# Kernel optimization log

Hardware: AMD Instinct MI355X
Metric: run time of the kernel (lower is better)

The kernel has to match this reference:

```python
import jax, jax.numpy as jnp
import numpy as np

B, L, D, H = 1024, 128, 768, 256
EPS = 1e-5  # torch BatchNorm1d default eps


def _masked_mean(x, lens):
    # x: [B, L, D], lens: [B] int -> mean over first lens[i] rows per sample
    mask = (jnp.arange(x.shape[1])[None, :] < lens[:, None]).astype(x.dtype)  # [B, L]
    return jnp.einsum('bld,bl->bd', x, mask) / lens[:, None].astype(x.dtype)


def _batchnorm_train(x, gamma, beta):
    # training-mode BN: batch mean and biased variance
    mu = jnp.mean(x, axis=0)
    var = jnp.mean((x - mu) ** 2, axis=0)
    return gamma * (x - mu) / jnp.sqrt(var + EPS) + beta


def setup_inputs() -> dict:
    key = jax.random.key(0)
    ks = jax.random.split(key, 12)
    user_features = jax.random.normal(ks[0], (B, L, D), jnp.float32)
    hashtag_features = jax.random.normal(ks[1], (B, L, D), jnp.float32)
    user_lens = jax.random.randint(ks[2], (B,), 1, L + 1, jnp.int32)
    hashtag_lens = jax.random.randint(ks[3], (B,), 1, L + 1, jnp.int32)
    def lin(k, fan_out, fan_in):
        bound = 1.0 / np.sqrt(fan_in)
        kw, kb = jax.random.split(k)
        w = jax.random.uniform(kw, (fan_out, fan_in), jnp.float32, -bound, bound)
        b = jax.random.uniform(kb, (fan_out,), jnp.float32, -bound, bound)
        return w, b
    fc1_w, fc1_b = lin(ks[4], D, 2 * D)
    fc2_w, fc2_b = lin(ks[5], H, D)
    fc3_w, fc3_b = lin(ks[6], 1, H)
    bn1_g = jnp.ones((D,), jnp.float32)
    bn1_b = jnp.zeros((D,), jnp.float32)
    bn2_g = jnp.ones((H,), jnp.float32)
    bn2_b = jnp.zeros((H,), jnp.float32)
    return {
        'user_features': user_features, 'hashtag_features': hashtag_features,
        'user_lens': user_lens, 'hashtag_lens': hashtag_lens,
        'fc1_w': fc1_w, 'fc1_b': fc1_b, 'bn1_g': bn1_g, 'bn1_b': bn1_b,
        'fc2_w': fc2_w, 'fc2_b': fc2_b, 'bn2_g': bn2_g, 'bn2_b': bn2_b,
        'fc3_w': fc3_w, 'fc3_b': fc3_b,
    }


def reference(user_features, hashtag_features, user_lens, hashtag_lens,
              fc1_w, fc1_b, bn1_g, bn1_b, fc2_w, fc2_b, bn2_g, bn2_b,
              fc3_w, fc3_b):
    # fused ragged mean pooling (replaces per-sample python loop)
    u = _masked_mean(user_features, user_lens)       # [B, D]
    h = _masked_mean(hashtag_features, hashtag_lens)  # [B, D]
    x = jnp.concatenate([u, h], axis=1)               # [B, 2D]
    x = jax.nn.relu(_batchnorm_train(x @ fc1_w.T + fc1_b, bn1_g, bn1_b))
    x = jax.nn.relu(_batchnorm_train(x @ fc2_w.T + fc2_b, bn2_g, bn2_b))
    out = jax.nn.sigmoid(x @ fc3_w.T + fc3_b)          # [B, 1]
    return out
```

## Files before the change

kernel.cpp:

```cpp
#include <hip/hip_runtime.h>
#include <cstdint>
#include <cstddef>

#define BATCH 1024
#define SEQL  128
#define DIM   768
#define HID   256
#define KIN1  1536
#define BN_EPS 1e-5f

typedef unsigned short u16;
typedef __attribute__((ext_vector_type(8))) short short8;
typedef __attribute__((ext_vector_type(4))) float f32x4;

__device__ __forceinline__ u16 f2bf(float f) {
  uint32_t u = __float_as_uint(f);
  return (u16)((u + 0x7fffu + ((u >> 16) & 1u)) >> 16);
}
__device__ __forceinline__ f32x4 ntl(const f32x4* p) { return __builtin_nontemporal_load(p); }
__device__ __forceinline__ float kred(float v) {
  v += __shfl_xor(v, 16);
  v += __shfl_xor(v, 32);
  return v;
}

__global__ __launch_bounds__(192) void pool_kernel(
    const float* __restrict__ uf, const float* __restrict__ hf,
    const int* __restrict__ ul, const int* __restrict__ hl,
    u16* __restrict__ xb) {
  const int b = blockIdx.x;
  const int which = blockIdx.y;
  const f32x4* src = (const f32x4*)((which ? hf : uf) + (size_t)b * (SEQL * DIM));
  const int len = which ? hl[b] : ul[b];
  const int t = threadIdx.x;

  f32x4 a0 = (f32x4){0.f, 0.f, 0.f, 0.f}, a1 = a0, a2 = a0, a3 = a0;
  int l = 0;
  for (; l + 8 <= len; l += 8) {
    f32x4 v0 = ntl(src + (size_t)(l + 0) * 192 + t);
    f32x4 v1 = ntl(src + (size_t)(l + 1) * 192 + t);
    f32x4 v2 = ntl(src + (size_t)(l + 2) * 192 + t);
    f32x4 v3 = ntl(src + (size_t)(l + 3) * 192 + t);
    f32x4 v4 = ntl(src + (size_t)(l + 4) * 192 + t);
    f32x4 v5 = ntl(src + (size_t)(l + 5) * 192 + t);
    f32x4 v6 = ntl(src + (size_t)(l + 6) * 192 + t);
    f32x4 v7 = ntl(src + (size_t)(l + 7) * 192 + t);
    a0 += v0; a1 += v1; a2 += v2; a3 += v3;
    a0 += v4; a1 += v5; a2 += v6; a3 += v7;
  }
  for (; l < len; ++l) a0 += ntl(src + (size_t)l * 192 + t);
  a0 += a1; a2 += a3; a0 += a2;
  const float s = 1.f / (float)len;
  ushort4 o = make_ushort4(f2bf(a0[0] * s), f2bf(a0[1] * s), f2bf(a0[2] * s), f2bf(a0[3] * s));
  *(ushort4*)(xb + (size_t)b * KIN1 + which * DIM + t * 4) = o;
}

__global__ __launch_bounds__(256) void prep_kernel(
    const float* __restrict__ w1, const float* __restrict__ w2,
    u16* __restrict__ w1b, u16* __restrict__ w2b) {
  const int n1 = DIM * KIN1 / 4;
  const int n2 = HID * DIM / 4;
  int i = blockIdx.x * 256 + threadIdx.x;
  if (i < n1) {
    f32x4 v = ((const f32x4*)w1)[i];
    ((ushort4*)w1b)[i] = make_ushort4(f2bf(v[0]), f2bf(v[1]), f2bf(v[2]), f2bf(v[3]));
  } else {
    i -= n1;
    if (i < n2) {
      f32x4 v = ((const f32x4*)w2)[i];
      ((ushort4*)w2b)[i] = make_ushort4(f2bf(v[0]), f2bf(v[1]), f2bf(v[2]), f2bf(v[3]));
    }
  }
}

#define LDT 72

__global__ __launch_bounds__(256) void gemm1_kernel(
    const u16* __restrict__ A, const u16* __restrict__ W,
    const float* __restrict__ bias, float* __restrict__ y, float* __restrict__ p1) {
  __shared__ u16 lA[64 * LDT];
  __shared__ u16 lB[64 * LDT];
  __shared__ float red[2][64][2];
  const int K = KIN1, N = DIM;
  const int tid = threadIdx.x, lane = tid & 63, wv = tid >> 6;
  const int wr = wv >> 1, wc = wv & 1;
  const int r16 = lane & 15, kgrp = lane >> 4;
  const int bm = blockIdx.x, bn = blockIdx.y;
  const int sr = tid >> 3, sc8 = (tid & 7) * 8;

  f32x4 acc[2][2];
#pragma unroll
  for (int mi = 0; mi < 2; ++mi)
#pragma unroll
    for (int ni = 0; ni < 2; ++ni) acc[mi][ni] = (f32x4){0.f, 0.f, 0.f, 0.f};

  const u16* Ab = A + (size_t)bm * 64 * K;
  const u16* Wb = W + (size_t)bn * 64 * K;

  for (int k0 = 0; k0 < K; k0 += 64) {
    uint4 ra0 = *(const uint4*)(Ab + (size_t)sr * K + k0 + sc8);
    uint4 ra1 = *(const uint4*)(Ab + (size_t)(sr + 32) * K + k0 + sc8);
    uint4 rb0 = *(const uint4*)(Wb + (size_t)sr * K + k0 + sc8);
    uint4 rb1 = *(const uint4*)(Wb + (size_t)(sr + 32) * K + k0 + sc8);
    __syncthreads();
    *(uint4*)(lA + sr * LDT + sc8) = ra0;
    *(uint4*)(lA + (sr + 32) * LDT + sc8) = ra1;
    *(uint4*)(lB + sr * LDT + sc8) = rb0;
    *(uint4*)(lB + (sr + 32) * LDT + sc8) = rb1;
    __syncthreads();
#pragma unroll
    for (int kk = 0; kk < 2; ++kk) {
      const int koff = (kk * 4 + kgrp) * 8;
      short8 af0 = *(const short8*)(lA + (wr * 32 + r16) * LDT + koff);
      short8 af1 = *(const short8*)(lA + (wr * 32 + 16 + r16) * LDT + koff);
      short8 bf0 = *(const short8*)(lB + (wc * 32 + r16) * LDT + koff);
      short8 bf1 = *(const short8*)(lB + (wc * 32 + 16 + r16) * LDT + koff);
      acc[0][0] = __builtin_amdgcn_mfma_f32_16x16x32_bf16(af0, bf0, acc[0][0], 0, 0, 0);
      acc[0][1] = __builtin_amdgcn_mfma_f32_16x16x32_bf16(af0, bf1, acc[0][1], 0, 0, 0);
      acc[1][0] = __builtin_amdgcn_mfma_f32_16x16x32_bf16(af1, bf0, acc[1][0], 0, 0, 0);
      acc[1][1] = __builtin_amdgcn_mfma_f32_16x16x32_bf16(af1, bf1, acc[1][1], 0, 0, 0);
    }
  }

#pragma unroll
  for (int ni = 0; ni < 2; ++ni) {
    const int col = bn * 64 + wc * 32 + ni * 16 + r16;
    const float bv = bias[col];
    float s = 0.f, s2 = 0.f;
#pragma unroll
    for (int mi = 0; mi < 2; ++mi)
#pragma unroll
      for (int rg = 0; rg < 4; ++rg) {
        const int row = bm * 64 + wr * 32 + mi * 16 + kgrp * 4 + rg;
        const float v = acc[mi][ni][rg] + bv;
        y[(size_t)row * N + col] = v;
        s += v; s2 += v * v;
      }
    s = kred(s); s2 = kred(s2);
    if (lane < 16) {
      red[wr][wc * 32 + ni * 16 + r16][0] = s;
      red[wr][wc * 32 + ni * 16 + r16][1] = s2;
    }
  }
  __syncthreads();
  if (tid < 128) {
    const int col = tid >> 1, wh = tid & 1;
    p1[((size_t)bm * DIM + bn * 64 + col) * 2 + wh] = red[0][col][wh] + red[1][col][wh];
  }
}

__global__ __launch_bounds__(256) void gemm2_kernel(
    const float* __restrict__ y1, const u16* __restrict__ W,
    const float* __restrict__ bias, const float* __restrict__ g, const float* __restrict__ be,
    const float* __restrict__ p1, float* __restrict__ y2, float* __restrict__ p2) {
  __shared__ u16 lA[64 * LDT];
  __shared__ u16 lB[32 * LDT];
  __shared__ float sS[DIM], sH[DIM];
  __shared__ float red[2][32][2];
  const int K = DIM, N = HID;
  const int tid = threadIdx.x, lane = tid & 63, wv = tid >> 6;
  const int wr = wv >> 1, wc = wv & 1;
  const int r16 = lane & 15, kgrp = lane >> 4;
  const int bm = blockIdx.x, bn = blockIdx.y;
  const int sr = tid >> 3, sc8 = (tid & 7) * 8;

  for (int c = tid; c < DIM; c += 256) {
    float s = 0.f, s2 = 0.f;
#pragma unroll
    for (int i = 0; i < 16; ++i) {
      float2 pv = *(const float2*)(p1 + ((size_t)i * DIM + c) * 2);
      s += pv.x; s2 += pv.y;
    }
    const float m = s * (1.f / BATCH);
    const float var = s2 * (1.f / BATCH) - m * m;
    const float r = rsqrtf(var + BN_EPS);
    const float scl = r * g[c];
    sS[c] = scl;
    sH[c] = be[c] - m * scl;
  }
  __syncthreads();

  f32x4 acc[2];
  acc[0] = (f32x4){0.f, 0.f, 0.f, 0.f};
  acc[1] = acc[0];

  const float* Ab = y1 + (size_t)bm * 64 * K;
  const u16* Wb = W + (size_t)bn * 32 * K;

  for (int k0 = 0; k0 < K; k0 += 64) {
    f32x4 va00 = *(const f32x4*)(Ab + (size_t)sr * K + k0 + sc8);
    f32x4 va01 = *(const f32x4*)(Ab + (size_t)sr * K + k0 + sc8 + 4);
    f32x4 va10 = *(const f32x4*)(Ab + (size_t)(sr + 32) * K + k0 + sc8);
    f32x4 va11 = *(const f32x4*)(Ab + (size_t)(sr + 32) * K + k0 + sc8 + 4);
    uint4 rb = *(const uint4*)(Wb + (size_t)sr * K + k0 + sc8);
    f32x4 s0 = *(const f32x4*)&sS[k0 + sc8];
    f32x4 s1 = *(const f32x4*)&sS[k0 + sc8 + 4];
    f32x4 h0 = *(const f32x4*)&sH[k0 + sc8];
    f32x4 h1 = *(const f32x4*)&sH[k0 + sc8 + 4];
    __syncthreads();
    union { ushort us[8]; uint4 q; } pk0, pk1;
#pragma unroll
    for (int j = 0; j < 4; ++j) {
      pk0.us[j]     = f2bf(fmaxf(0.f, va00[j] * s0[j] + h0[j]));
      pk0.us[4 + j] = f2bf(fmaxf(0.f, va01[j] * s1[j] + h1[j]));
      pk1.us[j]     = f2bf(fmaxf(0.f, va10[j] * s0[j] + h0[j]));
      pk1.us[4 + j] = f2bf(fmaxf(0.f, va11[j] * s1[j] + h1[j]));
    }
    *(uint4*)(lA + sr * LDT + sc8) = pk0.q;
    *(uint4*)(lA + (sr + 32) * LDT + sc8) = pk1.q;
    *(uint4*)(lB + sr * LDT + sc8) = rb;
    __syncthreads();
#pragma unroll
    for (int kk = 0; kk < 2; ++kk) {
      const int koff = (kk * 4 + kgrp) * 8;
      short8 af0 = *(const short8*)(lA + (wr * 32 + r16) * LDT + koff);
      short8 af1 = *(const short8*)(lA + (wr * 32 + 16 + r16) * LDT + koff);
      short8 bf0 = *(const short8*)(lB + (wc * 16 + r16) * LDT + koff);
      acc[0] = __builtin_amdgcn_mfma_f32_16x16x32_bf16(af0, bf0, acc[0], 0, 0, 0);
      acc[1] = __builtin_amdgcn_mfma_f32_16x16x32_bf16(af1, bf0, acc[1], 0, 0, 0);
    }
  }

  {
    const int col = bn * 32 + wc * 16 + r16;
    const float bv = bias[col];
    float s = 0.f, s2 = 0.f;
#pragma unroll
    for (int mi = 0; mi < 2; ++mi)
#pragma unroll
      for (int rg = 0; rg < 4; ++rg) {
        const int row = bm * 64 + wr * 32 + mi * 16 + kgrp * 4 + rg;
        const float v = acc[mi][rg] + bv;
        y2[(size_t)row * N + col] = v;
        s += v; s2 += v * v;
      }
    s = kred(s); s2 = kred(s2);
    if (lane < 16) {
      red[wr][wc * 16 + r16][0] = s;
      red[wr][wc * 16 + r16][1] = s2;
    }
  }
  __syncthreads();
  if (tid < 64) {
    const int col = tid >> 1, wh = tid & 1;
    p2[((size_t)bm * HID + bn * 32 + col) * 2 + wh] = red[0][col][wh] + red[1][col][wh];
  }
}

__global__ __launch_bounds__(256) void fc3_kernel(
    const float* __restrict__ y2, const float* __restrict__ p2,
    const float* __restrict__ g, const float* __restrict__ be,
    const float* __restrict__ w3, const float* __restrict__ b3, float* __restrict__ out) {
  __shared__ float sS[HID], sH[HID];
  const int tid = threadIdx.x;
  {
    const int c = tid;
    float s = 0.f, s2 = 0.f;
#pragma unroll
    for (int i = 0; i < 16; ++i) {
      float2 pv = *(const float2*)(p2 + ((size_t)i * HID + c) * 2);
      s += pv.x; s2 += pv.y;
    }
    const float m = s * (1.f / BATCH);
    const float var = s2 * (1.f / BATCH) - m * m;
    const float r = rsqrtf(var + BN_EPS);
    const float scl = r * g[c];
    sS[c] = scl;
    sH[c] = be[c] - m * scl;
  }
  __syncthreads();
  const int row = blockIdx.x * 4 + (tid >> 6);
  const int lane = tid & 63;
  f32x4 xv = *(const f32x4*)(y2 + (size_t)row * HID + lane * 4);
  f32x4 sc = *(const f32x4*)&sS[lane * 4];
  f32x4 sh = *(const f32x4*)&sH[lane * 4];
  f32x4 wv = *(const f32x4*)(w3 + lane * 4);
  float d = 0.f;
#pragma unroll
  for (int j = 0; j < 4; ++j) d += fmaxf(0.f, xv[j] * sc[j] + sh[j]) * wv[j];
#pragma unroll
  for (int off = 32; off > 0; off >>= 1) d += __shfl_xor(d, off);
  if (lane == 0) out[row] = 1.f / (1.f + expf(-(d + b3[0])));
}

extern "C" void kernel_launch(void* const* d_in, const int* in_sizes, int n_in,
                              void* d_out, int out_size, void* d_ws, size_t ws_size,
                              hipStream_t stream) {
  const float* uf   = (const float*)d_in[0];
  const float* hf   = (const float*)d_in[1];
  const int*   ul   = (const int*)d_in[2];
  const int*   hl   = (const int*)d_in[3];
  const float* fc1w = (const float*)d_in[4];
  const float* fc1b = (const float*)d_in[5];
  const float* bn1g = (const float*)d_in[6];
  const float* bn1b = (const float*)d_in[7];
  const float* fc2w = (const float*)d_in[8];
  const float* fc2b = (const float*)d_in[9];
  const float* bn2g = (const float*)d_in[10];
  const float* bn2b = (const float*)d_in[11];
  const float* fc3w = (const float*)d_in[12];
  const float* fc3b = (const float*)d_in[13];
  float* out = (float*)d_out;

  char* ws = (char*)d_ws;
  u16*   xb  = (u16*)  (ws + 0);
  u16*   w1b = (u16*)  (ws + 3145728);
  u16*   w2b = (u16*)  (ws + 5505024);
  float* y1  = (float*)(ws + 5898240);
  float* y2  = (float*)(ws + 9043968);
  float* p1  = (float*)(ws + 10092544);
  float* p2  = (float*)(ws + 10190848);

  pool_kernel<<<dim3(BATCH, 2), 192, 0, stream>>>(uf, hf, ul, hl, xb);
  prep_kernel<<<1344, 256, 0, stream>>>(fc1w, fc2w, w1b, w2b);
  gemm1_kernel<<<dim3(16, 12), 256, 0, stream>>>(xb, w1b, fc1b, y1, p1);
  gemm2_kernel<<<dim3(16, 8), 256, 0, stream>>>(y1, w2b, fc2b, bn1g, bn1b, p1, y2, p2);
  fc3_kernel<<<256, 256, 0, stream>>>(y2, p2, bn2g, bn2b, fc3w, fc3b, out);
}
```

Before: 118.5 us.

## Fuse pooling with weight prep, double-buffer GEMMs, remap blocks, shrink GEMM2 tiles

```diff
diff --git a/kernel.cpp b/kernel.cpp
--- a/kernel.cpp
+++ b/kernel.cpp
@@ -24,51 +24,55 @@
   return v;
 }
 
-__global__ __launch_bounds__(192) void pool_kernel(
+#define PREP_BLK 224
+#define NW1Q (DIM * KIN1 / 4)
+#define NWQ  (NW1Q + HID * DIM / 4)
+
+__global__ __launch_bounds__(192) void pool_prep_kernel(
     const float* __restrict__ uf, const float* __restrict__ hf,
     const int* __restrict__ ul, const int* __restrict__ hl,
-    u16* __restrict__ xb) {
-  const int b = blockIdx.x;
-  const int which = blockIdx.y;
-  const f32x4* src = (const f32x4*)((which ? hf : uf) + (size_t)b * (SEQL * DIM));
-  const int len = which ? hl[b] : ul[b];
+    const float* __restrict__ w1, const float* __restrict__ w2,
+    u16* __restrict__ xb, u16* __restrict__ w1b, u16* __restrict__ w2b) {
+  const int id = blockIdx.x;
   const int t = threadIdx.x;
-
-  f32x4 a0 = (f32x4){0.f, 0.f, 0.f, 0.f}, a1 = a0, a2 = a0, a3 = a0;
-  int l = 0;
-  for (; l + 8 <= len; l += 8) {
-    f32x4 v0 = ntl(src + (size_t)(l + 0) * 192 + t);
-    f32x4 v1 = ntl(src + (size_t)(l + 1) * 192 + t);
-    f32x4 v2 = ntl(src + (size_t)(l + 2) * 192 + t);
-    f32x4 v3 = ntl(src + (size_t)(l + 3) * 192 + t);
-    f32x4 v4 = ntl(src + (size_t)(l + 4) * 192 + t);
-    f32x4 v5 = ntl(src + (size_t)(l + 5) * 192 + t);
-    f32x4 v6 = ntl(src + (size_t)(l + 6) * 192 + t);
-    f32x4 v7 = ntl(src + (size_t)(l + 7) * 192 + t);
-    a0 += v0; a1 += v1; a2 += v2; a3 += v3;
-    a0 += v4; a1 += v5; a2 += v6; a3 += v7;
-  }
-  for (; l < len; ++l) a0 += ntl(src + (size_t)l * 192 + t);
-  a0 += a1; a2 += a3; a0 += a2;
-  const float s = 1.f / (float)len;
-  ushort4 o = make_ushort4(f2bf(a0[0] * s), f2bf(a0[1] * s), f2bf(a0[2] * s), f2bf(a0[3] * s));
-  *(ushort4*)(xb + (size_t)b * KIN1 + which * DIM + t * 4) = o;
-}
-
-__global__ __launch_bounds__(256) void prep_kernel(
-    const float* __restrict__ w1, const float* __restrict__ w2,
-    u16* __restrict__ w1b, u16* __restrict__ w2b) {
-  const int n1 = DIM * KIN1 / 4;
-  const int n2 = HID * DIM / 4;
-  int i = blockIdx.x * 256 + threadIdx.x;
-  if (i < n1) {
-    f32x4 v = ((const f32x4*)w1)[i];
-    ((ushort4*)w1b)[i] = make_ushort4(f2bf(v[0]), f2bf(v[1]), f2bf(v[2]), f2bf(v[3]));
+  if (id < 2048) {
+    const int b = id >> 1;
+    const int which = id & 1;
+    const f32x4* src = (const f32x4*)((which ? hf : uf) + (size_t)b * (SEQL * DIM));
+    const int len = which ? hl[b] : ul[b];
+    f32x4 a0 = (f32x4){0.f, 0.f, 0.f, 0.f}, a1 = a0, a2 = a0, a3 = a0;
+    int l = 0;
+    for (; l + 8 <= len; l += 8) {
+      f32x4 v0 = ntl(src + (size_t)(l + 0) * 192 + t);
+      f32x4 v1 = ntl(src + (size_t)(l + 1) * 192 + t);
+      f32x4 v2 = ntl(src + (size_t)(l + 2) * 192 + t);
+      f32x4 v3 = ntl(src + (size_t)(l + 3) * 192 + t);
+      f32x4 v4 = ntl(src + (size_t)(l + 4) * 192 + t);
+      f32x4 v5 = ntl(src + (size_t)(l + 5) * 192 + t);
+      f32x4 v6 = ntl(src + (size_t)(l + 6) * 192 + t);
+      f32x4 v7 = ntl(src + (size_t)(l + 7) * 192 + t);
+      a0 += v0; a1 += v1; a2 += v2; a3 += v3;
+      a0 += v4; a1 += v5; a2 += v6; a3 += v7;
+    }
+    for (; l < len; ++l) a0 += ntl(src + (size_t)l * 192 + t);
+    a0 += a1; a2 += a3; a0 += a2;
+    const float s = 1.f / (float)len;
+    ushort4 o = make_ushort4(f2bf(a0[0] * s), f2bf(a0[1] * s), f2bf(a0[2] * s), f2bf(a0[3] * s));
+    *(ushort4*)(xb + (size_t)b * KIN1 + which * DIM + t * 4) = o;
   } else {
-    i -= n1;
-    if (i < n2) {
-      f32x4 v = ((const f32x4*)w2)[i];
-      ((ushort4*)w2b)[i] = make_ushort4(f2bf(v[0]), f2bf(v[1]), f2bf(v[2]), f2bf(v[3]));
+    const int j = id - 2048;
+    const int base = j * 192 + t;
+#pragma unroll
+    for (int s = 0; s < 8; ++s) {
+      const int i = base + s * (PREP_BLK * 192);
+      if (i < NW1Q) {
+        f32x4 v = ((const f32x4*)w1)[i];
+        ((ushort4*)w1b)[i] = make_ushort4(f2bf(v[0]), f2bf(v[1]), f2bf(v[2]), f2bf(v[3]));
+      } else {
+        const int i2 = i - NW1Q;
+        f32x4 v = ((const f32x4*)w2)[i2];
+        ((ushort4*)w2b)[i2] = make_ushort4(f2bf(v[0]), f2bf(v[1]), f2bf(v[2]), f2bf(v[3]));
+      }
     }
   }
 }
@@ -78,14 +82,17 @@
 __global__ __launch_bounds__(256) void gemm1_kernel(
     const u16* __restrict__ A, const u16* __restrict__ W,
     const float* __restrict__ bias, float* __restrict__ y, float* __restrict__ p1) {
-  __shared__ u16 lA[64 * LDT];
-  __shared__ u16 lB[64 * LDT];
+  __shared__ u16 lA[2][64 * LDT];
+  __shared__ u16 lB[2][64 * LDT];
   __shared__ float red[2][64][2];
   const int K = KIN1, N = DIM;
   const int tid = threadIdx.x, lane = tid & 63, wv = tid >> 6;
   const int wr = wv >> 1, wc = wv & 1;
   const int r16 = lane & 15, kgrp = lane >> 4;
-  const int bm = blockIdx.x, bn = blockIdx.y;
+  const int d = blockIdx.x;
+  const int g = d & 7, j = d >> 3;
+  const int bm = (g >> 1) * 4 + (j & 3);
+  const int bn = (g & 1) * 6 + (j >> 2);
   const int sr = tid >> 3, sc8 = (tid & 7) * 8;
 
   f32x4 acc[2][2];
@@ -97,29 +104,40 @@
   const u16* Ab = A + (size_t)bm * 64 * K;
   const u16* Wb = W + (size_t)bn * 64 * K;
 
-  for (int k0 = 0; k0 < K; k0 += 64) {
-    uint4 ra0 = *(const uint4*)(Ab + (size_t)sr * K + k0 + sc8);
-    uint4 ra1 = *(const uint4*)(Ab + (size_t)(sr + 32) * K + k0 + sc8);
-    uint4 rb0 = *(const uint4*)(Wb + (size_t)sr * K + k0 + sc8);
-    uint4 rb1 = *(const uint4*)(Wb + (size_t)(sr + 32) * K + k0 + sc8);
-    __syncthreads();
-    *(uint4*)(lA + sr * LDT + sc8) = ra0;
-    *(uint4*)(lA + (sr + 32) * LDT + sc8) = ra1;
-    *(uint4*)(lB + sr * LDT + sc8) = rb0;
-    *(uint4*)(lB + (sr + 32) * LDT + sc8) = rb1;
-    __syncthreads();
+  uint4 ra0, ra1, rb0, rb1;
+#define G1_LOAD(k0)                                              \
+  ra0 = *(const uint4*)(Ab + (size_t)sr * K + (k0) + sc8);       \
+  ra1 = *(const uint4*)(Ab + (size_t)(sr + 32) * K + (k0) + sc8);\
+  rb0 = *(const uint4*)(Wb + (size_t)sr * K + (k0) + sc8);       \
+  rb1 = *(const uint4*)(Wb + (size_t)(sr + 32) * K + (k0) + sc8);
+#define G1_WRITE(buf)                                \
+  *(uint4*)(lA[buf] + sr * LDT + sc8) = ra0;         \
+  *(uint4*)(lA[buf] + (sr + 32) * LDT + sc8) = ra1;  \
+  *(uint4*)(lB[buf] + sr * LDT + sc8) = rb0;         \
+  *(uint4*)(lB[buf] + (sr + 32) * LDT + sc8) = rb1;
+
+  G1_LOAD(0)
+  G1_WRITE(0)
+  __syncthreads();
+  const int nk = K / 64;
+  for (int ti = 0; ti < nk; ++ti) {
+    const int cur = ti & 1;
+    const bool more = (ti + 1 < nk);
+    if (more) { G1_LOAD((ti + 1) * 64) }
 #pragma unroll
     for (int kk = 0; kk < 2; ++kk) {
       const int koff = (kk * 4 + kgrp) * 8;
-      short8 af0 = *(const short8*)(lA + (wr * 32 + r16) * LDT + koff);
-      short8 af1 = *(const short8*)(lA + (wr * 32 + 16 + r16) * LDT + koff);
-      short8 bf0 = *(const short8*)(lB + (wc * 32 + r16) * LDT + koff);
-      short8 bf1 = *(const short8*)(lB + (wc * 32 + 16 + r16) * LDT + koff);
+      short8 af0 = *(const short8*)(lA[cur] + (wr * 32 + r16) * LDT + koff);
+      short8 af1 = *(const short8*)(lA[cur] + (wr * 32 + 16 + r16) * LDT + koff);
+      short8 bf0 = *(const short8*)(lB[cur] + (wc * 32 + r16) * LDT + koff);
+      short8 bf1 = *(const short8*)(lB[cur] + (wc * 32 + 16 + r16) * LDT + koff);
       acc[0][0] = __builtin_amdgcn_mfma_f32_16x16x32_bf16(af0, bf0, acc[0][0], 0, 0, 0);
       acc[0][1] = __builtin_amdgcn_mfma_f32_16x16x32_bf16(af0, bf1, acc[0][1], 0, 0, 0);
       acc[1][0] = __builtin_amdgcn_mfma_f32_16x16x32_bf16(af1, bf0, acc[1][0], 0, 0, 0);
       acc[1][1] = __builtin_amdgcn_mfma_f32_16x16x32_bf16(af1, bf1, acc[1][1], 0, 0, 0);
     }
+    if (more) { G1_WRITE(cur ^ 1) }
+    __syncthreads();
   }
 
 #pragma unroll
@@ -153,15 +171,18 @@
     const float* __restrict__ y1, const u16* __restrict__ W,
     const float* __restrict__ bias, const float* __restrict__ g, const float* __restrict__ be,
     const float* __restrict__ p1, float* __restrict__ y2, float* __restrict__ p2) {
-  __shared__ u16 lA[64 * LDT];
-  __shared__ u16 lB[32 * LDT];
+  __shared__ u16 lA[2][32 * LDT];
+  __shared__ u16 lB[2][32 * LDT];
   __shared__ float sS[DIM], sH[DIM];
   __shared__ float red[2][32][2];
   const int K = DIM, N = HID;
   const int tid = threadIdx.x, lane = tid & 63, wv = tid >> 6;
   const int wr = wv >> 1, wc = wv & 1;
   const int r16 = lane & 15, kgrp = lane >> 4;
-  const int bm = blockIdx.x, bn = blockIdx.y;
+  const int d = blockIdx.x;
+  const int g8 = d & 7, j = d >> 3;
+  const int bm = g8 * 4 + (j & 3);
+  const int bn = j >> 2;
   const int sr = tid >> 3, sc8 = (tid & 7) * 8;
 
   for (int c = tid; c < DIM; c += 256) {
@@ -180,45 +201,45 @@
   }
   __syncthreads();
 
-  f32x4 acc[2];
-  acc[0] = (f32x4){0.f, 0.f, 0.f, 0.f};
-  acc[1] = acc[0];
-
-  const float* Ab = y1 + (size_t)bm * 64 * K;
+  f32x4 acc = (f32x4){0.f, 0.f, 0.f, 0.f};
+  const float* Ab = y1 + (size_t)bm * 32 * K;
   const u16* Wb = W + (size_t)bn * 32 * K;
 
-  for (int k0 = 0; k0 < K; k0 += 64) {
-    f32x4 va00 = *(const f32x4*)(Ab + (size_t)sr * K + k0 + sc8);
-    f32x4 va01 = *(const f32x4*)(Ab + (size_t)sr * K + k0 + sc8 + 4);
-    f32x4 va10 = *(const f32x4*)(Ab + (size_t)(sr + 32) * K + k0 + sc8);
-    f32x4 va11 = *(const f32x4*)(Ab + (size_t)(sr + 32) * K + k0 + sc8 + 4);
-    uint4 rb = *(const uint4*)(Wb + (size_t)sr * K + k0 + sc8);
-    f32x4 s0 = *(const f32x4*)&sS[k0 + sc8];
-    f32x4 s1 = *(const f32x4*)&sS[k0 + sc8 + 4];
-    f32x4 h0 = *(const f32x4*)&sH[k0 + sc8];
-    f32x4 h1 = *(const f32x4*)&sH[k0 + sc8 + 4];
-    __syncthreads();
-    union { ushort us[8]; uint4 q; } pk0, pk1;
-#pragma unroll
-    for (int j = 0; j < 4; ++j) {
-      pk0.us[j]     = f2bf(fmaxf(0.f, va00[j] * s0[j] + h0[j]));
-      pk0.us[4 + j] = f2bf(fmaxf(0.f, va01[j] * s1[j] + h1[j]));
-      pk1.us[j]     = f2bf(fmaxf(0.f, va10[j] * s0[j] + h0[j]));
-      pk1.us[4 + j] = f2bf(fmaxf(0.f, va11[j] * s1[j] + h1[j]));
-    }
-    *(uint4*)(lA + sr * LDT + sc8) = pk0.q;
-    *(uint4*)(lA + (sr + 32) * LDT + sc8) = pk1.q;
-    *(uint4*)(lB + sr * LDT + sc8) = rb;
-    __syncthreads();
+  f32x4 va0, va1;
+  uint4 rbq;
+#define G2_LOAD(k0)                                          \
+  va0 = *(const f32x4*)(Ab + (size_t)sr * K + (k0) + sc8);   \
+  va1 = *(const f32x4*)(Ab + (size_t)sr * K + (k0) + sc8 + 4);\
+  rbq = *(const uint4*)(Wb + (size_t)sr * K + (k0) + sc8);
+
+  auto pack_write = [&](int buf, int k0) {
+    union { ushort us[8]; uint4 q; } pk;
+#pragma unroll
+    for (int jj = 0; jj < 4; ++jj) {
+      pk.us[jj]     = f2bf(fmaxf(0.f, va0[jj] * sS[k0 + sc8 + jj] + sH[k0 + sc8 + jj]));
+      pk.us[4 + jj] = f2bf(fmaxf(0.f, va1[jj] * sS[k0 + sc8 + 4 + jj] + sH[k0 + sc8 + 4 + jj]));
+    }
+    *(uint4*)(lA[buf] + sr * LDT + sc8) = pk.q;
+    *(uint4*)(lB[buf] + sr * LDT + sc8) = rbq;
+  };
+
+  G2_LOAD(0)
+  pack_write(0, 0);
+  __syncthreads();
+  const int nk = K / 64;
+  for (int ti = 0; ti < nk; ++ti) {
+    const int cur = ti & 1;
+    const bool more = (ti + 1 < nk);
+    if (more) { G2_LOAD((ti + 1) * 64) }
 #pragma unroll
     for (int kk = 0; kk < 2; ++kk) {
       const int koff = (kk * 4 + kgrp) * 8;
-      short8 af0 = *(const short8*)(lA + (wr * 32 + r16) * LDT + koff);
-      short8 af1 = *(const short8*)(lA + (wr * 32 + 16 + r16) * LDT + koff);
-      short8 bf0 = *(const short8*)(lB + (wc * 16 + r16) * LDT + koff);
-      acc[0] = __builtin_amdgcn_mfma_f32_16x16x32_bf16(af0, bf0, acc[0], 0, 0, 0);
-      acc[1] = __builtin_amdgcn_mfma_f32_16x16x32_bf16(af1, bf0, acc[1], 0, 0, 0);
-    }
+      short8 af0 = *(const short8*)(lA[cur] + (wr * 16 + r16) * LDT + koff);
+      short8 bf0 = *(const short8*)(lB[cur] + (wc * 16 + r16) * LDT + koff);
+      acc = __builtin_amdgcn_mfma_f32_16x16x32_bf16(af0, bf0, acc, 0, 0, 0);
+    }
+    if (more) pack_write(cur ^ 1, (ti + 1) * 64);
+    __syncthreads();
   }
 
   {
@@ -226,14 +247,12 @@
     const float bv = bias[col];
     float s = 0.f, s2 = 0.f;
 #pragma unroll
-    for (int mi = 0; mi < 2; ++mi)
-#pragma unroll
-      for (int rg = 0; rg < 4; ++rg) {
-        const int row = bm * 64 + wr * 32 + mi * 16 + kgrp * 4 + rg;
-        const float v = acc[mi][rg] + bv;
-        y2[(size_t)row * N + col] = v;
-        s += v; s2 += v * v;
-      }
+    for (int rg = 0; rg < 4; ++rg) {
+      const int row = bm * 32 + wr * 16 + kgrp * 4 + rg;
+      const float v = acc[rg] + bv;
+      y2[(size_t)row * N + col] = v;
+      s += v; s2 += v * v;
+    }
     s = kred(s); s2 = kred(s2);
     if (lane < 16) {
       red[wr][wc * 16 + r16][0] = s;
@@ -257,7 +276,7 @@
     const int c = tid;
     float s = 0.f, s2 = 0.f;
 #pragma unroll
-    for (int i = 0; i < 16; ++i) {
+    for (int i = 0; i < 32; ++i) {
       float2 pv = *(const float2*)(p2 + ((size_t)i * HID + c) * 2);
       s += pv.x; s2 += pv.y;
     }
@@ -275,12 +294,12 @@
   f32x4 sc = *(const f32x4*)&sS[lane * 4];
   f32x4 sh = *(const f32x4*)&sH[lane * 4];
   f32x4 wv = *(const f32x4*)(w3 + lane * 4);
-  float d = 0.f;
-#pragma unroll
-  for (int j = 0; j < 4; ++j) d += fmaxf(0.f, xv[j] * sc[j] + sh[j]) * wv[j];
-#pragma unroll
-  for (int off = 32; off > 0; off >>= 1) d += __shfl_xor(d, off);
-  if (lane == 0) out[row] = 1.f / (1.f + expf(-(d + b3[0])));
+  float dsum = 0.f;
+#pragma unroll
+  for (int jj = 0; jj < 4; ++jj) dsum += fmaxf(0.f, xv[jj] * sc[jj] + sh[jj]) * wv[jj];
+#pragma unroll
+  for (int off = 32; off > 0; off >>= 1) dsum += __shfl_xor(dsum, off);
+  if (lane == 0) out[row] = 1.f / (1.f + expf(-(dsum + b3[0])));
 }
 
 extern "C" void kernel_launch(void* const* d_in, const int* in_sizes, int n_in,
@@ -311,9 +330,8 @@
   float* p1  = (float*)(ws + 10092544);
   float* p2  = (float*)(ws + 10190848);
 
-  pool_kernel<<<dim3(BATCH, 2), 192, 0, stream>>>(uf, hf, ul, hl, xb);
-  prep_kernel<<<1344, 256, 0, stream>>>(fc1w, fc2w, w1b, w2b);
-  gemm1_kernel<<<dim3(16, 12), 256, 0, stream>>>(xb, w1b, fc1b, y1, p1);
-  gemm2_kernel<<<dim3(16, 8), 256, 0, stream>>>(y1, w2b, fc2b, bn1g, bn1b, p1, y2, p2);
+  pool_prep_kernel<<<2048 + PREP_BLK, 192, 0, stream>>>(uf, hf, ul, hl, fc1w, fc2w, xb, w1b, w2b);
+  gemm1_kernel<<<192, 256, 0, stream>>>(xb, w1b, fc1b, y1, p1);
+  gemm2_kernel<<<256, 256, 0, stream>>>(y1, w2b, fc2b, bn1g, bn1b, p1, y2, p2);
   fc3_kernel<<<256, 256, 0, stream>>>(y2, p2, bn2g, bn2b, fc3w, fc3b, out);
 }
```

Measured after the change: 112.5 us. -5.0%, faster.
